# Performance work log

Hardware: AMD Instinct MI355X
Metric: run time of the kernel (lower is better)

Reference implementation:

```python
import jax, jax.numpy as jnp
import numpy as np

B, H, W, C = 64, 56, 56, 96
NH, WS, SS = 3, 7, 3
HID = 4 * C
N = WS * WS              # tokens per window = 49
NW = (H // WS) * (W // WS)  # windows per image = 64
HD = C // NH             # head dim = 32
SCALE = HD ** -0.5


def _rel_pos_index():
    coords = np.stack(np.meshgrid(np.arange(WS), np.arange(WS), indexing='ij'))  # (2, WS, WS)
    cf = coords.reshape(2, -1)                      # (2, N)
    rel = cf[:, :, None] - cf[:, None, :]           # (2, N, N)
    rel = rel.transpose(1, 2, 0)                    # (N, N, 2)
    rel[:, :, 0] += WS - 1
    rel[:, :, 1] += WS - 1
    rel[:, :, 0] *= 2 * WS - 1
    return rel.sum(-1)                              # (N, N) int


def _attn_mask():
    # shift-window mask per original Swin: label regions, mask cross-region pairs with -100
    img = np.zeros((H, W))
    cnt = 0
    sl = (slice(0, -WS), slice(-WS, -SS), slice(-SS, None))
    for hs in sl:
        for ws_ in sl:
            img[hs, ws_] = cnt
            cnt += 1
    mw = img.reshape(H // WS, WS, W // WS, WS).transpose(0, 2, 1, 3).reshape(-1, N)  # (NW, N)
    am = mw[:, None, :] - mw[:, :, None]
    return np.where(am != 0, -100.0, 0.0).astype(np.float32)  # (NW, N, N)


REL_IDX = jnp.asarray(_rel_pos_index())
ATTN_MASK = jnp.asarray(_attn_mask())


def _ln(x, g, b):
    m = x.mean(-1, keepdims=True)
    v = x.var(-1, keepdims=True)
    return (x - m) / jnp.sqrt(v + 1e-5) * g + b


def setup_inputs() -> dict:
    key = jax.random.key(0)
    ks = jax.random.split(key, 8)
    s = lambda k, shape: jax.random.normal(k, shape, jnp.float32) * 0.02
    return dict(
        x=jax.random.normal(ks[0], (B, H * W, C), jnp.float32),
        norm1_g=jnp.ones((C,), jnp.float32), norm1_b=jnp.zeros((C,), jnp.float32),
        qkv_w=s(ks[1], (3 * C, C)), qkv_b=jnp.zeros((3 * C,), jnp.float32),
        rpb_table=s(ks[2], ((2 * WS - 1) ** 2, NH)),
        proj_w=s(ks[3], (C, C)), proj_b=jnp.zeros((C,), jnp.float32),
        norm2_g=jnp.ones((C,), jnp.float32), norm2_b=jnp.zeros((C,), jnp.float32),
        fc1_w=s(ks[4], (HID, C)), fc1_b=jnp.zeros((HID,), jnp.float32),
        fc2_w=s(ks[5], (C, HID)), fc2_b=jnp.zeros((C,), jnp.float32),
    )


def reference(x, norm1_g, norm1_b, qkv_w, qkv_b, rpb_table, proj_w, proj_b,
              norm2_g, norm2_b, fc1_w, fc1_b, fc2_w, fc2_b):
    shortcut = x                                    # (B, H*W, C)
    h = _ln(x, norm1_g, norm1_b).reshape(B, H, W, C)
    # cyclic shift for SW-MSA
    h = jnp.roll(h, (-SS, -SS), axis=(1, 2))
    # window partition -> (B*NW, N, C)
    hw = h.reshape(B, H // WS, WS, W // WS, WS, C).transpose(0, 1, 3, 2, 4, 5).reshape(B * NW, N, C)
    # qkv projection
    qkv = (hw @ qkv_w.T + qkv_b).reshape(B * NW, N, 3, NH, HD).transpose(2, 0, 3, 1, 4)
    q, k, v = qkv[0] * SCALE, qkv[1], qkv[2]        # each (B*NW, NH, N, HD)
    attn = jnp.einsum('bhnd,bhmd->bhnm', q, k)      # (B*NW, NH, N, N)
    # relative position bias gather: (N, N, NH) -> (NH, N, N)
    bias = rpb_table[REL_IDX].transpose(2, 0, 1)
    attn = attn + bias[None]
    # shift mask: broadcast over batch and heads
    attn = attn.reshape(B, NW, NH, N, N) + ATTN_MASK[None, :, None]
    attn = jax.nn.softmax(attn.reshape(B * NW, NH, N, N), axis=-1)
    out = jnp.einsum('bhnm,bhmd->bhnd', attn, v).transpose(0, 2, 1, 3).reshape(B * NW, N, C)
    out = out @ proj_w.T + proj_b
    # window reverse + reverse shift
    out = out.reshape(B, H // WS, W // WS, WS, WS, C).transpose(0, 1, 3, 2, 4, 5).reshape(B, H, W, C)
    out = jnp.roll(out, (SS, SS), axis=(1, 2)).reshape(B, H * W, C)
    x = shortcut + out
    # MLP with residual (erf-based GELU, matching torch nn.GELU default)
    h2 = _ln(x, norm2_g, norm2_b)
    h2 = jax.nn.gelu(h2 @ fc1_w.T + fc1_b, approximate=False) @ fc2_w.T + fc2_b
    return x + h2
```

## Files before the change

### kernel.cpp

```cpp
#include <hip/hip_runtime.h>
#include <math.h>

#define BB   64
#define HH   56
#define WWD  56
#define CCH  96
#define SSS  3
#define NTK  49
#define TOKENS (BB*HH*WWD)

typedef unsigned short ushort;
typedef short short8 __attribute__((ext_vector_type(8)));
typedef float floatx4 __attribute__((ext_vector_type(4)));

__device__ __forceinline__ ushort f2bf(float f) {
    union { float f; unsigned u; } v; v.f = f;
    unsigned r = v.u + 0x7FFF + ((v.u >> 16) & 1);
    return (ushort)(r >> 16);
}

__device__ __forceinline__ float fast_gelu(float v) {
    float u = v * (1.5957691216f + 0.071354816f * (v * v));
    float r = __builtin_amdgcn_rcpf(__expf(u) + 1.f);
    return v - v * r;
}

#define WQKV  0
#define WPROJ (54*512)
#define WFC1  (72*512)
#define WFC2  (144*512)
#define NFRAG 216

__global__ __launch_bounds__(256) void wconv(
    const float* __restrict__ qkv_w, const float* __restrict__ proj_w,
    const float* __restrict__ fc1_w, const float* __restrict__ fc2_w,
    ushort* __restrict__ wsb)
{
    int tg = blockIdx.x * 256 + threadIdx.x;
    int frag = tg >> 6, lane = tg & 63, l15 = lane & 15, quad = lane >> 4;
    const float* src; int row, kbase, K;
    if (frag < 54)       { int f = frag;       int ct = f/3,  kt = f%3;  src = qkv_w;  row = ct*16+l15; kbase = kt*32+quad*8; K = 96;  }
    else if (frag < 72)  { int f = frag - 54;  int ct = f/3,  kt = f%3;  src = proj_w; row = ct*16+l15; kbase = kt*32+quad*8; K = 96;  }
    else if (frag < 144) { int f = frag - 72;  int ct = f/3,  kt = f%3;  src = fc1_w;  row = ct*16+l15; kbase = kt*32+quad*8; K = 96;  }
    else                 { int f = frag - 144; int ct = f/12, hc = f%12; src = fc2_w;  row = ct*16+l15; kbase = hc*32+quad*8; K = 384; }
    const float* p = src + (size_t)row * K + kbase;
    ushort tmp[8];
    #pragma unroll
    for (int j = 0; j < 8; ++j) tmp[j] = f2bf(p[j]);
    *(short8*)(wsb + (size_t)frag * 512 + lane * 8) = *(const short8*)tmp;
}

__global__ __launch_bounds__(256, 3) void swin_kernel(
    const float* __restrict__ x,
    const float* __restrict__ n1g, const float* __restrict__ n1b,
    const ushort* __restrict__ wsb,
    const float* __restrict__ qkv_b, const float* __restrict__ rpb,
    const float* __restrict__ proj_b,
    const float* __restrict__ n2g, const float* __restrict__ n2b,
    const float* __restrict__ fc1_b, const float* __restrict__ fc2_b,
    float* __restrict__ out)
{
    __shared__ ushort xa[64][104];
    __shared__ float  kvf[6592];
    __shared__ ushort ps[64][72];
    __shared__ float  rpbs[507];

    ushort (*ks)[104] = (ushort(*)[104])kvf;
    ushort (*vt)[68]  = (ushort(*)[68])((ushort*)kvf + 64*104);

    const int wgid = blockIdx.x;
    const int b  = wgid >> 6;
    const int wy = (wgid >> 3) & 7;
    const int wx = wgid & 7;
    const int tid  = threadIdx.x;
    const int lane = tid & 63;
    const int wv   = tid >> 6;
    const int l15  = lane & 15;
    const int quad = lane >> 4;
    const int m0   = wv * 16;

    for (int i = tid; i < 507; i += 256) rpbs[i] = rpb[i];

    {
        float g0 = n1g[lane], bb0 = n1b[lane];
        float g1 = (lane < 32) ? n1g[64 + lane] : 0.f;
        float bb1 = (lane < 32) ? n1b[64 + lane] : 0.f;
        for (int r16 = 0; r16 < 16; ++r16) {
            int t = m0 + r16;
            if (t < NTK) {
                int yi = t / 7, xi = t % 7;
                int rr = wy * 7 + yi + SSS; if (rr >= HH)  rr -= HH;
                int cc = wx * 7 + xi + SSS; if (cc >= WWD) cc -= WWD;
                const float* px = x + ((size_t)(b * HH + rr) * WWD + cc) * CCH;
                float v0 = px[lane];
                float v1 = (lane < 32) ? px[64 + lane] : 0.f;
                float s = v0 + v1;
                float q = v0 * v0 + v1 * v1;
                #pragma unroll
                for (int o = 32; o; o >>= 1) { s += __shfl_xor(s, o); q += __shfl_xor(q, o); }
                float mean = s * (1.f / 96.f);
                float rstd = rsqrtf(q * (1.f / 96.f) - mean * mean + 1e-5f);
                xa[t][lane] = f2bf((v0 - mean) * rstd * g0 + bb0);
                if (lane < 32) xa[t][64 + lane] = f2bf((v1 - mean) * rstd * g1 + bb1);
            } else {
                xa[t][lane] = 0;
                if (lane < 32) xa[t][64 + lane] = 0;
            }
        }
    }

    float qreg[6][4];
    for (int ct = 0; ct < 18; ++ct) {
        floatx4 acc = {0.f, 0.f, 0.f, 0.f};
        #pragma unroll
        for (int kt = 0; kt < 3; ++kt) {
            short8 a  = *(const short8*)&xa[m0 + l15][kt * 32 + quad * 8];
            short8 bw = *(const short8*)(wsb + WQKV + (size_t)(ct * 3 + kt) * 512 + lane * 8);
            acc = __builtin_amdgcn_mfma_f32_16x16x32_bf16(a, bw, acc, 0, 0, 0);
        }
        int oc = ct * 16 + l15;
        float bias = qkv_b[oc];
        if (ct < 6) {
            #pragma unroll
            for (int r = 0; r < 4; ++r) qreg[ct][r] = (acc[r] + bias) * 0.17677669529663687f;
        } else if (ct < 12) {
            #pragma unroll
            for (int r = 0; r < 4; ++r) ks[m0 + quad * 4 + r][oc - 96] = f2bf(acc[r] + bias);
        } else {
            #pragma unroll
            for (int r = 0; r < 4; ++r) vt[oc - 192][m0 + quad * 4 + r] = f2bf(acc[r] + bias);
        }
    }
    #pragma unroll
    for (int ct = 0; ct < 6; ++ct)
        #pragma unroll
        for (int r = 0; r < 4; ++r)
            xa[m0 + quad * 4 + r][ct * 16 + l15] = f2bf(qreg[ct][r]);
    short8 aq[3];
    #pragma unroll
    for (int h = 0; h < 3; ++h) aq[h] = *(const short8*)&xa[m0 + l15][h * 32 + quad * 8];
    __syncthreads();

    int rowm[4], rowy[4], rowx[4], rowli[4];
    #pragma unroll
    for (int r = 0; r < 4; ++r) {
        int m = m0 + quad * 4 + r;
        rowm[r] = m;
        int yi = m / 7, xi = m - 7 * yi;
        rowy[r] = yi; rowx[r] = xi;
        int ri = wy * 7 + yi, ci = wx * 7 + xi;
        rowli[r] = (ri < 49 ? 0 : (ri < 53 ? 1 : 2)) * 3 + (ci < 49 ? 0 : (ci < 53 ? 1 : 2));
    }
    int gofs[4];
    #pragma unroll
    for (int r = 0; r < 4; ++r) {
        int rr = wy * 7 + rowy[r] + SSS; if (rr >= HH)  rr -= HH;
        int cc = wx * 7 + rowx[r] + SSS; if (cc >= WWD) cc -= WWD;
        gofs[r] = ((b * HH + rr) * WWD + cc) * CCH;
    }
    int   rix3[4][4];
    float badd[4][4];
    #pragma unroll
    for (int ct = 0; ct < 4; ++ct) {
        int cj = ct * 16 + l15;
        int cok = cj < NTK;
        int yj = cj / 7, xj = cj - 7 * yj;
        int rj = wy * 7 + yj, cjc = wx * 7 + xj;
        int lj = (rj < 49 ? 0 : (rj < 53 ? 1 : 2)) * 3 + (cjc < 49 ? 0 : (cjc < 53 ? 1 : 2));
        #pragma unroll
        for (int r = 0; r < 4; ++r) {
            int ok = cok && (rowm[r] < NTK);
            int ridx = ok ? (rowy[r] - yj + 6) * 13 + (rowx[r] - xj + 6) : 0;
            rix3[ct][r] = ridx * 3;
            badd[ct][r] = !ok ? -1e30f : (rowli[r] != lj ? -100.f : 0.f);
        }
    }

    for (int h = 0; h < 3; ++h) {
        const int hb = 32 * h;
        float sc0[4][4];
        #pragma unroll
        for (int ct = 0; ct < 4; ++ct) {
            short8 bk = *(const short8*)&ks[ct * 16 + l15][hb + quad * 8];
            floatx4 acc = {0.f, 0.f, 0.f, 0.f};
            acc = __builtin_amdgcn_mfma_f32_16x16x32_bf16(aq[h], bk, acc, 0, 0, 0);
            #pragma unroll
            for (int r = 0; r < 4; ++r)
                sc0[ct][r] = acc[r] + rpbs[rix3[ct][r] + h] + badd[ct][r];
        }
        #pragma unroll
        for (int r = 0; r < 4; ++r) {
            float mx = fmaxf(fmaxf(sc0[0][r], sc0[1][r]), fmaxf(sc0[2][r], sc0[3][r]));
            #pragma unroll
            for (int o = 1; o < 16; o <<= 1) mx = fmaxf(mx, __shfl_xor(mx, o));
            float sum = 0.f;
            #pragma unroll
            for (int ct = 0; ct < 4; ++ct) { float e = __expf(sc0[ct][r] - mx); sc0[ct][r] = e; sum += e; }
            #pragma unroll
            for (int o = 1; o < 16; o <<= 1) sum += __shfl_xor(sum, o);
            float inv = __builtin_amdgcn_rcpf(sum);
            #pragma unroll
            for (int ct = 0; ct < 4; ++ct)
                ps[rowm[r]][ct * 16 + l15] = f2bf(sc0[ct][r] * inv);
        }
        short8 ap0 = *(const short8*)&ps[m0 + l15][quad * 8];
        short8 ap1 = *(const short8*)&ps[m0 + l15][32 + quad * 8];
        #pragma unroll
        for (int nt = 0; nt < 2; ++nt) {
            floatx4 acc = {0.f, 0.f, 0.f, 0.f};
            short8 bv0 = *(const short8*)&vt[hb + nt * 16 + l15][quad * 8];
            short8 bv1 = *(const short8*)&vt[hb + nt * 16 + l15][32 + quad * 8];
            acc = __builtin_amdgcn_mfma_f32_16x16x32_bf16(ap0, bv0, acc, 0, 0, 0);
            acc = __builtin_amdgcn_mfma_f32_16x16x32_bf16(ap1, bv1, acc, 0, 0, 0);
            #pragma unroll
            for (int r = 0; r < 4; ++r)
                xa[m0 + quad * 4 + r][hb + nt * 16 + l15] = f2bf(acc[r]);
        }
    }

    __syncthreads();

    float xrv[6][4];
    for (int ct = 0; ct < 6; ++ct) {
        floatx4 acc = {0.f, 0.f, 0.f, 0.f};
        #pragma unroll
        for (int kt = 0; kt < 3; ++kt) {
            short8 a  = *(const short8*)&xa[m0 + l15][kt * 32 + quad * 8];
            short8 bw = *(const short8*)(wsb + WPROJ + (size_t)(ct * 3 + kt) * 512 + lane * 8);
            acc = __builtin_amdgcn_mfma_f32_16x16x32_bf16(a, bw, acc, 0, 0, 0);
        }
        int c2 = ct * 16 + l15;
        float pb = proj_b[c2];
        #pragma unroll
        for (int r = 0; r < 4; ++r) {
            float v = 0.f;
            if (rowm[r] < NTK) v = acc[r] + pb + x[gofs[r] + c2];
            xrv[ct][r] = v;
        }
    }

    float gn[6], bn[6];
    #pragma unroll
    for (int ct = 0; ct < 6; ++ct) { gn[ct] = n2g[ct * 16 + l15]; bn[ct] = n2b[ct * 16 + l15]; }
    #pragma unroll
    for (int r = 0; r < 4; ++r) {
        float s = 0.f, q = 0.f;
        #pragma unroll
        for (int ct = 0; ct < 6; ++ct) { s += xrv[ct][r]; q += xrv[ct][r] * xrv[ct][r]; }
        #pragma unroll
        for (int o = 1; o < 16; o <<= 1) { s += __shfl_xor(s, o); q += __shfl_xor(q, o); }
        float mean = s * (1.f / 96.f);
        float rstd = rsqrtf(q * (1.f / 96.f) - mean * mean + 1e-5f);
        #pragma unroll
        for (int ct = 0; ct < 6; ++ct)
            xa[m0 + quad * 4 + r][ct * 16 + l15] =
                f2bf((xrv[ct][r] - mean) * rstd * gn[ct] + bn[ct]);
    }

    short8 axn[3];
    #pragma unroll
    for (int kt = 0; kt < 3; ++kt) axn[kt] = *(const short8*)&xa[m0 + l15][kt * 32 + quad * 8];
    ushort* actb = (ushort*)kvf + wv * 1280;
    floatx4 o2[6];
    #pragma unroll
    for (int ct = 0; ct < 6; ++ct) o2[ct] = (floatx4){0.f, 0.f, 0.f, 0.f};

    short8 aprev;
    for (int hc = 0; hc < 12; ++hc) {
        floatx4 a1[2];
        #pragma unroll
        for (int c2t = 0; c2t < 2; ++c2t) {
            floatx4 acc = {0.f, 0.f, 0.f, 0.f};
            #pragma unroll
            for (int kt = 0; kt < 3; ++kt) {
                short8 bw = *(const short8*)(wsb + WFC1 + (size_t)((hc * 2 + c2t) * 3 + kt) * 512 + lane * 8);
                acc = __builtin_amdgcn_mfma_f32_16x16x32_bf16(axn[kt], bw, acc, 0, 0, 0);
            }
            a1[c2t] = acc;
        }
        if (hc > 0)
            aprev = *(const short8*)(actb + ((hc - 1) & 1) * 640 + l15 * 40 + quad * 8);
        #pragma unroll
        for (int c2t = 0; c2t < 2; ++c2t) {
            float b1 = fc1_b[(hc * 2 + c2t) * 16 + l15];
            #pragma unroll
            for (int r = 0; r < 4; ++r) {
                float g = fast_gelu(a1[c2t][r] + b1);
                actb[(hc & 1) * 640 + (quad * 4 + r) * 40 + c2t * 16 + l15] = f2bf(g);
            }
        }
        if (hc > 0) {
            #pragma unroll
            for (int ct = 0; ct < 6; ++ct) {
                short8 bw = *(const short8*)(wsb + WFC2 + (size_t)(ct * 12 + hc - 1) * 512 + lane * 8);
                o2[ct] = __builtin_amdgcn_mfma_f32_16x16x32_bf16(aprev, bw, o2[ct], 0, 0, 0);
            }
        }
    }
    aprev = *(const short8*)(actb + 640 + l15 * 40 + quad * 8);
    #pragma unroll
    for (int ct = 0; ct < 6; ++ct) {
        short8 bw = *(const short8*)(wsb + WFC2 + (size_t)(ct * 12 + 11) * 512 + lane * 8);
        o2[ct] = __builtin_amdgcn_mfma_f32_16x16x32_bf16(aprev, bw, o2[ct], 0, 0, 0);
    }

    for (int ct = 0; ct < 6; ++ct) {
        int c = ct * 16 + l15;
        float b2 = fc2_b[c];
        #pragma unroll
        for (int r = 0; r < 4; ++r) {
            if (rowm[r] >= NTK) continue;
            out[gofs[r] + c] = xrv[ct][r] + o2[ct][r] + b2;
        }
    }
}

extern "C" void kernel_launch(void* const* d_in, const int* in_sizes, int n_in,
                              void* d_out, int out_size, void* d_ws, size_t ws_size,
                              hipStream_t stream) {
    const float* x      = (const float*)d_in[0];
    const float* n1g    = (const float*)d_in[1];
    const float* n1b    = (const float*)d_in[2];
    const float* qkv_w  = (const float*)d_in[3];
    const float* qkv_b  = (const float*)d_in[4];
    const float* rpb    = (const float*)d_in[5];
    const float* proj_w = (const float*)d_in[6];
    const float* proj_b = (const float*)d_in[7];
    const float* n2g    = (const float*)d_in[8];
    const float* n2b    = (const float*)d_in[9];
    const float* fc1_w  = (const float*)d_in[10];
    const float* fc1_b  = (const float*)d_in[11];
    const float* fc2_w  = (const float*)d_in[12];
    const float* fc2_b  = (const float*)d_in[13];
    float* out = (float*)d_out;
    ushort* wsb = (ushort*)d_ws;

    wconv<<<NFRAG / 4, 256, 0, stream>>>(qkv_w, proj_w, fc1_w, fc2_w, wsb);
    swin_kernel<<<BB * 64, 256, 0, stream>>>(
        x, n1g, n1b, wsb, qkv_b, rpb, proj_b, n2g, n2b, fc1_b, fc2_b, out);
}
```

Before: 429.1 us.

## Compute transposed attention scores and shuffle probabilities in registers, shrinking LDS

The QK^T MFMA now computes the transposed score tile (keys by queries), so the softmax reduces mostly within each thread and needs only two cross-lane shuffles. The probabilities are packed to bf16 and rearranged into the PV A-operand layout with lane shuffles, which removes the ps LDS buffer and its round trip. Padding on the xa and ks rows is reduced, and LayerNorm1 is rewritten in the MFMA row layout, so less LDS is used per block and launch bounds can rise to 4 blocks per CU. The tighter register budget may cause spills, and the narrower row padding may add LDS bank conflicts.

```diff
diff --git a/kernel.cpp b/kernel.cpp
--- a/kernel.cpp
+++ b/kernel.cpp
@@ -50,7 +50,7 @@
     *(short8*)(wsb + (size_t)frag * 512 + lane * 8) = *(const short8*)tmp;
 }
 
-__global__ __launch_bounds__(256, 3) void swin_kernel(
+__global__ __launch_bounds__(256, 4) void swin_kernel(
     const float* __restrict__ x,
     const float* __restrict__ n1g, const float* __restrict__ n1b,
     const ushort* __restrict__ wsb,
@@ -60,13 +60,12 @@
     const float* __restrict__ fc1_b, const float* __restrict__ fc2_b,
     float* __restrict__ out)
 {
-    __shared__ ushort xa[64][104];
-    __shared__ float  kvf[6592];
-    __shared__ ushort ps[64][72];
+    __shared__ ushort xa[64][100];
+    __shared__ float  kvf[6464];
     __shared__ float  rpbs[507];
 
-    ushort (*ks)[104] = (ushort(*)[104])kvf;
-    ushort (*vt)[68]  = (ushort(*)[68])((ushort*)kvf + 64*104);
+    ushort (*ks)[100] = (ushort(*)[100])kvf;
+    ushort (*vt)[68]  = (ushort(*)[68])((ushort*)kvf + 64*100);
 
     const int wgid = blockIdx.x;
     const int b  = wgid >> 6;
@@ -81,67 +80,7 @@
 
     for (int i = tid; i < 507; i += 256) rpbs[i] = rpb[i];
 
-    {
-        float g0 = n1g[lane], bb0 = n1b[lane];
-        float g1 = (lane < 32) ? n1g[64 + lane] : 0.f;
-        float bb1 = (lane < 32) ? n1b[64 + lane] : 0.f;
-        for (int r16 = 0; r16 < 16; ++r16) {
-            int t = m0 + r16;
-            if (t < NTK) {
-                int yi = t / 7, xi = t % 7;
-                int rr = wy * 7 + yi + SSS; if (rr >= HH)  rr -= HH;
-                int cc = wx * 7 + xi + SSS; if (cc >= WWD) cc -= WWD;
-                const float* px = x + ((size_t)(b * HH + rr) * WWD + cc) * CCH;
-                float v0 = px[lane];
-                float v1 = (lane < 32) ? px[64 + lane] : 0.f;
-                float s = v0 + v1;
-                float q = v0 * v0 + v1 * v1;
-                #pragma unroll
-                for (int o = 32; o; o >>= 1) { s += __shfl_xor(s, o); q += __shfl_xor(q, o); }
-                float mean = s * (1.f / 96.f);
-                float rstd = rsqrtf(q * (1.f / 96.f) - mean * mean + 1e-5f);
-                xa[t][lane] = f2bf((v0 - mean) * rstd * g0 + bb0);
-                if (lane < 32) xa[t][64 + lane] = f2bf((v1 - mean) * rstd * g1 + bb1);
-            } else {
-                xa[t][lane] = 0;
-                if (lane < 32) xa[t][64 + lane] = 0;
-            }
-        }
-    }
-
-    float qreg[6][4];
-    for (int ct = 0; ct < 18; ++ct) {
-        floatx4 acc = {0.f, 0.f, 0.f, 0.f};
-        #pragma unroll
-        for (int kt = 0; kt < 3; ++kt) {
-            short8 a  = *(const short8*)&xa[m0 + l15][kt * 32 + quad * 8];
-            short8 bw = *(const short8*)(wsb + WQKV + (size_t)(ct * 3 + kt) * 512 + lane * 8);
-            acc = __builtin_amdgcn_mfma_f32_16x16x32_bf16(a, bw, acc, 0, 0, 0);
-        }
-        int oc = ct * 16 + l15;
-        float bias = qkv_b[oc];
-        if (ct < 6) {
-            #pragma unroll
-            for (int r = 0; r < 4; ++r) qreg[ct][r] = (acc[r] + bias) * 0.17677669529663687f;
-        } else if (ct < 12) {
-            #pragma unroll
-            for (int r = 0; r < 4; ++r) ks[m0 + quad * 4 + r][oc - 96] = f2bf(acc[r] + bias);
-        } else {
-            #pragma unroll
-            for (int r = 0; r < 4; ++r) vt[oc - 192][m0 + quad * 4 + r] = f2bf(acc[r] + bias);
-        }
-    }
-    #pragma unroll
-    for (int ct = 0; ct < 6; ++ct)
-        #pragma unroll
-        for (int r = 0; r < 4; ++r)
-            xa[m0 + quad * 4 + r][ct * 16 + l15] = f2bf(qreg[ct][r]);
-    short8 aq[3];
-    #pragma unroll
-    for (int h = 0; h < 3; ++h) aq[h] = *(const short8*)&xa[m0 + l15][h * 32 + quad * 8];
-    __syncthreads();
-
-    int rowm[4], rowy[4], rowx[4], rowli[4];
+    int rowm[4], rowy[4], rowx[4], rowli[4], gofs[4];
     #pragma unroll
     for (int r = 0; r < 4; ++r) {
         int m = m0 + quad * 4 + r;
@@ -150,71 +89,154 @@
         rowy[r] = yi; rowx[r] = xi;
         int ri = wy * 7 + yi, ci = wx * 7 + xi;
         rowli[r] = (ri < 49 ? 0 : (ri < 53 ? 1 : 2)) * 3 + (ci < 49 ? 0 : (ci < 53 ? 1 : 2));
-    }
-    int gofs[4];
-    #pragma unroll
-    for (int r = 0; r < 4; ++r) {
-        int rr = wy * 7 + rowy[r] + SSS; if (rr >= HH)  rr -= HH;
-        int cc = wx * 7 + rowx[r] + SSS; if (cc >= WWD) cc -= WWD;
+        int rr = ri + SSS; if (rr >= HH)  rr -= HH;
+        int cc = ci + SSS; if (cc >= WWD) cc -= WWD;
         gofs[r] = ((b * HH + rr) * WWD + cc) * CCH;
     }
-    int   rix3[4][4];
-    float badd[4][4];
+
+    {
+        float gn1[6], bn1[6];
+        #pragma unroll
+        for (int ct = 0; ct < 6; ++ct) { gn1[ct] = n1g[ct*16+l15]; bn1[ct] = n1b[ct*16+l15]; }
+        #pragma unroll
+        for (int r = 0; r < 4; ++r) {
+            float xv[6];
+            if (rowm[r] < NTK) {
+                #pragma unroll
+                for (int ct = 0; ct < 6; ++ct) xv[ct] = x[gofs[r] + ct*16 + l15];
+            } else {
+                #pragma unroll
+                for (int ct = 0; ct < 6; ++ct) xv[ct] = 0.f;
+            }
+            float s = 0.f, q = 0.f;
+            #pragma unroll
+            for (int ct = 0; ct < 6; ++ct) { s += xv[ct]; q += xv[ct] * xv[ct]; }
+            #pragma unroll
+            for (int o = 1; o < 16; o <<= 1) { s += __shfl_xor(s, o); q += __shfl_xor(q, o); }
+            float mean = s * (1.f / 96.f);
+            float rstd = rsqrtf(q * (1.f / 96.f) - mean * mean + 1e-5f);
+            #pragma unroll
+            for (int ct = 0; ct < 6; ++ct)
+                xa[rowm[r]][ct*16 + l15] = f2bf((xv[ct] - mean) * rstd * gn1[ct] + bn1[ct]);
+        }
+    }
+
+    float qreg[6][4];
+    for (int ct = 0; ct < 18; ++ct) {
+        floatx4 acc = {0.f, 0.f, 0.f, 0.f};
+        #pragma unroll
+        for (int kt = 0; kt < 3; ++kt) {
+            short8 a  = *(const short8*)&xa[m0 + l15][kt * 32 + quad * 8];
+            short8 bw = *(const short8*)(wsb + WQKV + (size_t)(ct * 3 + kt) * 512 + lane * 8);
+            acc = __builtin_amdgcn_mfma_f32_16x16x32_bf16(a, bw, acc, 0, 0, 0);
+        }
+        int oc = ct * 16 + l15;
+        float bias = qkv_b[oc];
+        if (ct < 6) {
+            #pragma unroll
+            for (int r = 0; r < 4; ++r) qreg[ct][r] = (acc[r] + bias) * 0.17677669529663687f;
+        } else if (ct < 12) {
+            #pragma unroll
+            for (int r = 0; r < 4; ++r) ks[m0 + quad * 4 + r][oc - 96] = f2bf(acc[r] + bias);
+        } else {
+            #pragma unroll
+            for (int r = 0; r < 4; ++r) vt[oc - 192][m0 + quad * 4 + r] = f2bf(acc[r] + bias);
+        }
+    }
+    #pragma unroll
+    for (int ct = 0; ct < 6; ++ct)
+        #pragma unroll
+        for (int r = 0; r < 4; ++r)
+            xa[m0 + quad * 4 + r][ct * 16 + l15] = f2bf(qreg[ct][r]);
+    short8 aq[3];
+    #pragma unroll
+    for (int h = 0; h < 3; ++h) aq[h] = *(const short8*)&xa[m0 + l15][h * 32 + quad * 8];
+    __syncthreads();
+
+    int ql = m0 + l15;
+    int qy = ql / 7, qx = ql - 7 * qy;
+    int rq = wy * 7 + qy, cq = wx * 7 + qx;
+    int lq = (rq < 49 ? 0 : (rq < 53 ? 1 : 2)) * 3 + (cq < 49 ? 0 : (cq < 53 ? 1 : 2));
+    int qok = ql < NTK;
+    int rixT[4][4]; float baddT[4][4];
     #pragma unroll
     for (int ct = 0; ct < 4; ++ct) {
-        int cj = ct * 16 + l15;
-        int cok = cj < NTK;
-        int yj = cj / 7, xj = cj - 7 * yj;
-        int rj = wy * 7 + yj, cjc = wx * 7 + xj;
-        int lj = (rj < 49 ? 0 : (rj < 53 ? 1 : 2)) * 3 + (cjc < 49 ? 0 : (cjc < 53 ? 1 : 2));
         #pragma unroll
         for (int r = 0; r < 4; ++r) {
-            int ok = cok && (rowm[r] < NTK);
-            int ridx = ok ? (rowy[r] - yj + 6) * 13 + (rowx[r] - xj + 6) : 0;
-            rix3[ct][r] = ridx * 3;
-            badd[ct][r] = !ok ? -1e30f : (rowli[r] != lj ? -100.f : 0.f);
-        }
-    }
+            int k = ct * 16 + quad * 4 + r;
+            int ky = k / 7, kx = k - 7 * ky;
+            int rk = wy * 7 + ky, ck = wx * 7 + kx;
+            int lk = (rk < 49 ? 0 : (rk < 53 ? 1 : 2)) * 3 + (ck < 49 ? 0 : (ck < 53 ? 1 : 2));
+            int ok = qok && (k < NTK);
+            rixT[ct][r] = (ok ? ((qy - ky + 6) * 13 + (qx - kx + 6)) : 0) * 3;
+            baddT[ct][r] = !ok ? -1e30f : (lq != lk ? -100.f : 0.f);
+        }
+    }
+
+    const int s0 = ((quad & 1) << 5) + l15;
+    const int s1 = s0 + 16;
+    const bool hisel = quad >= 2;
 
     for (int h = 0; h < 3; ++h) {
         const int hb = 32 * h;
-        float sc0[4][4];
+        float st[4][4];
         #pragma unroll
         for (int ct = 0; ct < 4; ++ct) {
-            short8 bk = *(const short8*)&ks[ct * 16 + l15][hb + quad * 8];
+            short8 ak = *(const short8*)&ks[ct * 16 + l15][hb + quad * 8];
             floatx4 acc = {0.f, 0.f, 0.f, 0.f};
-            acc = __builtin_amdgcn_mfma_f32_16x16x32_bf16(aq[h], bk, acc, 0, 0, 0);
+            acc = __builtin_amdgcn_mfma_f32_16x16x32_bf16(ak, aq[h], acc, 0, 0, 0);
             #pragma unroll
             for (int r = 0; r < 4; ++r)
-                sc0[ct][r] = acc[r] + rpbs[rix3[ct][r] + h] + badd[ct][r];
-        }
-        #pragma unroll
-        for (int r = 0; r < 4; ++r) {
-            float mx = fmaxf(fmaxf(sc0[0][r], sc0[1][r]), fmaxf(sc0[2][r], sc0[3][r]));
-            #pragma unroll
-            for (int o = 1; o < 16; o <<= 1) mx = fmaxf(mx, __shfl_xor(mx, o));
-            float sum = 0.f;
-            #pragma unroll
-            for (int ct = 0; ct < 4; ++ct) { float e = __expf(sc0[ct][r] - mx); sc0[ct][r] = e; sum += e; }
-            #pragma unroll
-            for (int o = 1; o < 16; o <<= 1) sum += __shfl_xor(sum, o);
-            float inv = __builtin_amdgcn_rcpf(sum);
-            #pragma unroll
-            for (int ct = 0; ct < 4; ++ct)
-                ps[rowm[r]][ct * 16 + l15] = f2bf(sc0[ct][r] * inv);
-        }
-        short8 ap0 = *(const short8*)&ps[m0 + l15][quad * 8];
-        short8 ap1 = *(const short8*)&ps[m0 + l15][32 + quad * 8];
+                st[ct][r] = acc[r] + rpbs[rixT[ct][r] + h] + baddT[ct][r];
+        }
+        float mx = st[0][0];
+        #pragma unroll
+        for (int ct = 0; ct < 4; ++ct)
+            #pragma unroll
+            for (int r = 0; r < 4; ++r) mx = fmaxf(mx, st[ct][r]);
+        mx = fmaxf(mx, __shfl_xor(mx, 16));
+        mx = fmaxf(mx, __shfl_xor(mx, 32));
+        float sum = 0.f;
+        #pragma unroll
+        for (int ct = 0; ct < 4; ++ct)
+            #pragma unroll
+            for (int r = 0; r < 4; ++r) { float e = __expf(st[ct][r] - mx); st[ct][r] = e; sum += e; }
+        sum += __shfl_xor(sum, 16);
+        sum += __shfl_xor(sum, 32);
+        float inv = __builtin_amdgcn_rcpf(sum);
+        unsigned pk[4][2];
+        #pragma unroll
+        for (int ct = 0; ct < 4; ++ct) {
+            pk[ct][0] = (unsigned)f2bf(st[ct][0] * inv) | ((unsigned)f2bf(st[ct][1] * inv) << 16);
+            pk[ct][1] = (unsigned)f2bf(st[ct][2] * inv) | ((unsigned)f2bf(st[ct][3] * inv) << 16);
+        }
+        unsigned p00a = __shfl(pk[0][0], s0), p01a = __shfl(pk[0][1], s0);
+        unsigned p00b = __shfl(pk[0][0], s1), p01b = __shfl(pk[0][1], s1);
+        unsigned p10a = __shfl(pk[1][0], s0), p11a = __shfl(pk[1][1], s0);
+        unsigned p10b = __shfl(pk[1][0], s1), p11b = __shfl(pk[1][1], s1);
+        unsigned p20a = __shfl(pk[2][0], s0), p21a = __shfl(pk[2][1], s0);
+        unsigned p20b = __shfl(pk[2][0], s1), p21b = __shfl(pk[2][1], s1);
+        unsigned p30a = __shfl(pk[3][0], s0), p31a = __shfl(pk[3][1], s0);
+        unsigned p30b = __shfl(pk[3][0], s1), p31b = __shfl(pk[3][1], s1);
+        union { unsigned u[4]; short8 v; } a0, a1;
+        a0.u[0] = hisel ? p10a : p00a;
+        a0.u[1] = hisel ? p11a : p01a;
+        a0.u[2] = hisel ? p10b : p00b;
+        a0.u[3] = hisel ? p11b : p01b;
+        a1.u[0] = hisel ? p30a : p20a;
+        a1.u[1] = hisel ? p31a : p21a;
+        a1.u[2] = hisel ? p30b : p20b;
+        a1.u[3] = hisel ? p31b : p21b;
         #pragma unroll
         for (int nt = 0; nt < 2; ++nt) {
             floatx4 acc = {0.f, 0.f, 0.f, 0.f};
             short8 bv0 = *(const short8*)&vt[hb + nt * 16 + l15][quad * 8];
             short8 bv1 = *(const short8*)&vt[hb + nt * 16 + l15][32 + quad * 8];
-            acc = __builtin_amdgcn_mfma_f32_16x16x32_bf16(ap0, bv0, acc, 0, 0, 0);
-            acc = __builtin_amdgcn_mfma_f32_16x16x32_bf16(ap1, bv1, acc, 0, 0, 0);
+            acc = __builtin_amdgcn_mfma_f32_16x16x32_bf16(a0.v, bv0, acc, 0, 0, 0);
+            acc = __builtin_amdgcn_mfma_f32_16x16x32_bf16(a1.v, bv1, acc, 0, 0, 0);
             #pragma unroll
             for (int r = 0; r < 4; ++r)
-                xa[m0 + quad * 4 + r][hb + nt * 16 + l15] = f2bf(acc[r]);
+                xa[rowm[r]][hb + nt * 16 + l15] = f2bf(acc[r]);
         }
     }
 
@@ -253,7 +275,7 @@
         float rstd = rsqrtf(q * (1.f / 96.f) - mean * mean + 1e-5f);
         #pragma unroll
         for (int ct = 0; ct < 6; ++ct)
-            xa[m0 + quad * 4 + r][ct * 16 + l15] =
+            xa[rowm[r]][ct * 16 + l15] =
                 f2bf((xrv[ct][r] - mean) * rstd * gn[ct] + bn[ct]);
     }
 
@@ -267,7 +289,7 @@
 
     short8 aprev;
     for (int hc = 0; hc < 12; ++hc) {
-        floatx4 a1[2];
+        floatx4 a1c[2];
         #pragma unroll
         for (int c2t = 0; c2t < 2; ++c2t) {
             floatx4 acc = {0.f, 0.f, 0.f, 0.f};
@@ -276,7 +298,7 @@
                 short8 bw = *(const short8*)(wsb + WFC1 + (size_t)((hc * 2 + c2t) * 3 + kt) * 512 + lane * 8);
                 acc = __builtin_amdgcn_mfma_f32_16x16x32_bf16(axn[kt], bw, acc, 0, 0, 0);
             }
-            a1[c2t] = acc;
+            a1c[c2t] = acc;
         }
         if (hc > 0)
             aprev = *(const short8*)(actb + ((hc - 1) & 1) * 640 + l15 * 40 + quad * 8);
@@ -285,7 +307,7 @@
             float b1 = fc1_b[(hc * 2 + c2t) * 16 + l15];
             #pragma unroll
             for (int r = 0; r < 4; ++r) {
-                float g = fast_gelu(a1[c2t][r] + b1);
+                float g = fast_gelu(a1c[c2t][r] + b1);
                 actb[(hc & 1) * 640 + (quad * 4 + r) * 40 + c2t * 16 + l15] = f2bf(g);
             }
         }
```

New measurement: 382.3 us. -10.9%, faster.
